# Performance work log

Measured on AMD Instinct MI355X. Metric: run time of the kernel, lower is better.

The kernel has to match this reference:

```python
import jax, jax.numpy as jnp
import numpy as np

B, T, C, H = 4, 4096, 512, 64

def setup_inputs() -> dict:
    key = jax.random.key(0)
    kx, kk, kq, kv = jax.random.split(key, 4)
    return {
        "x": jax.random.normal(kx, (B, T, C), dtype=jnp.float32),
        "Wk": jax.random.normal(kk, (C, H), dtype=jnp.float32) * (C ** -0.5),
        "Wq": jax.random.normal(kq, (C, H), dtype=jnp.float32) * (C ** -0.5),
        "Wv": jax.random.normal(kv, (C, H), dtype=jnp.float32) * (C ** -0.5),
    }

def reference(x, Wk, Wq, Wv):
    # x: [B, T, C]; bias-free projections to head_size H
    k = x @ Wk  # [B, T, H]
    q = x @ Wq  # [B, T, H]
    v = x @ Wv  # [B, T, H]
    channels = x.shape[-1]
    # NOTE: original scales by channels**-0.5 (embedding dim), not head_size
    scale = jnp.asarray(channels, x.dtype) ** -0.5
    wei = jnp.einsum("bth,bsh->bts", q, k) * scale  # [B, T, T]
    t = x.shape[1]
    causal = jnp.tril(jnp.ones((t, t), dtype=bool))
    wei = jnp.where(causal, wei, -jnp.inf)
    wei = jax.nn.softmax(wei, axis=-1)
    out = jnp.einsum("bts,bsh->bth", wei, v)  # [B, T, H]
    return out
```

## Files before the change

kernel.cpp:

```cpp
#include <hip/hip_runtime.h>


typedef __attribute__((ext_vector_type(8))) __bf16 bf16x8;
typedef __attribute__((ext_vector_type(8))) unsigned short u16x8;
typedef __attribute__((ext_vector_type(4))) float f32x4;

#define B_ 4
#define T_ 4096
#define C_ 512
#define H_ 64
#define BT (B_ * T_)

#define QSCALE (0.04419417382415922f * 1.4426950408889634f)

__device__ __forceinline__ unsigned short f2bf(float f) {
    unsigned int u = __builtin_bit_cast(unsigned int, f);
    u += 0x7fffu + ((u >> 16) & 1u);
    return (unsigned short)(u >> 16);
}

__device__ __forceinline__ unsigned int pkbf(float hi, float lo) {
    return __builtin_amdgcn_perm(__builtin_bit_cast(unsigned int, hi),
                                 __builtin_bit_cast(unsigned int, lo), 0x07060302u);
}

__device__ __forceinline__ f32x4 mfma16(bf16x8 a, bf16x8 b, f32x4 c) {
    return __builtin_amdgcn_mfma_f32_16x16x32_bf16(a, b, c, 0, 0, 0);
}

__global__ __launch_bounds__(256) void wt_kernel(const float* __restrict__ Wk,
                                                 const float* __restrict__ Wq,
                                                 const float* __restrict__ Wv,
                                                 unsigned short* __restrict__ Wtp) {
    int gid = blockIdx.x * 256 + threadIdx.x;
    int fidx = gid >> 9;
    int li = gid & 511;
    int lane = li >> 3, j = li & 7;
    int m3 = fidx / 64;
    int rem = fidx & 63;
    int nt = rem >> 4, kc = rem & 15;
    int h = nt * 16 + (lane & 15);
    int c = kc * 32 + (lane >> 4) * 8 + j;
    const float* W = (m3 == 0) ? Wk : ((m3 == 1) ? Wq : Wv);
    Wtp[gid] = f2bf(W[c * H_ + h]);
}

__global__ __launch_bounds__(256, 4) void proj_kernel(const float* __restrict__ x,
                                                      const unsigned short* __restrict__ Wtp,
                                                      unsigned short* __restrict__ Kf,
                                                      unsigned short* __restrict__ Qf,
                                                      unsigned short* __restrict__ Vf) {
    __shared__ __align__(16) char smem[3 * 64 * 52 * 4];
    float* Mg = (float*)smem;
    unsigned short* Ks_l = (unsigned short*)smem;
    unsigned short* Qs_l = Ks_l + 16 * 68;
    unsigned short* Vt_l = Qs_l + 16 * 68;

    const int tid = threadIdx.x;
    const int t0 = blockIdx.x * 16;
    const int wave = tid >> 6;
    const int lane = tid & 63;
    const int lane15 = lane & 15;
    const int quad = lane >> 4;

    f32x4 acc[12];
#pragma unroll
    for (int i = 0; i < 12; ++i) acc[i] = (f32x4){0.f, 0.f, 0.f, 0.f};

    const float* xrow = x + (long)(t0 + lane15) * C_;

#pragma unroll
    for (int kk = 0; kk < 4; ++kk) {
        const int kc = wave * 4 + kk;
        const float4 a0 = *(const float4*)(xrow + kc * 32 + quad * 8);
        const float4 a1 = *(const float4*)(xrow + kc * 32 + quad * 8 + 4);
        u16x8 t;
        t[0] = f2bf(a0.x); t[1] = f2bf(a0.y); t[2] = f2bf(a0.z); t[3] = f2bf(a0.w);
        t[4] = f2bf(a1.x); t[5] = f2bf(a1.y); t[6] = f2bf(a1.z); t[7] = f2bf(a1.w);
        bf16x8 a = __builtin_bit_cast(bf16x8, t);
#pragma unroll
        for (int m3 = 0; m3 < 3; ++m3) {
#pragma unroll
            for (int nt = 0; nt < 4; ++nt) {
                const bf16x8 b = *(const bf16x8*)&Wtp[(((m3 * 4 + nt) * 16 + kc) << 9) + lane * 8];
                acc[m3 * 4 + nt] = mfma16(a, b, acc[m3 * 4 + nt]);
            }
        }
    }

    if (wave > 0) {
        float* mg = Mg + ((wave - 1) * 64 + lane) * 52;
#pragma unroll
        for (int i = 0; i < 12; ++i) *(f32x4*)(mg + i * 4) = acc[i];
    }
    __syncthreads();
    if (wave == 0) {
#pragma unroll
        for (int w = 0; w < 3; ++w) {
            const float* mg = Mg + (w * 64 + lane) * 52;
#pragma unroll
            for (int i = 0; i < 12; ++i) acc[i] += *(const f32x4*)(mg + i * 4);
        }
    }
    __syncthreads();

    if (wave == 0) {
#pragma unroll
        for (int nt = 0; nt < 4; ++nt) {
            int col = nt * 16 + lane15;
#pragma unroll
            for (int r = 0; r < 4; ++r) {
                int row_l = quad * 4 + r;
                Ks_l[row_l * 68 + col] = f2bf(acc[0 * 4 + nt][r]);
                Qs_l[row_l * 68 + col] = f2bf(acc[1 * 4 + nt][r] * QSCALE);
                Vt_l[col * 18 + row_l] = f2bf(acc[2 * 4 + nt][r]);
            }
        }
    }
    __syncthreads();

    const int b = t0 >> 12;
    const int tloc = t0 & 4095;
    const long gs = (long)(b * 256 + (tloc >> 4));

    {
        const unsigned short* src = (wave < 2) ? Ks_l : Qs_l;
        unsigned short* dst = (wave < 2) ? Kf : Qf;
        const int kk = wave & 1;
        bf16x8 v = *(const bf16x8*)&src[lane15 * 68 + kk * 32 + quad * 8];
        *(bf16x8*)&dst[(gs * 2 + kk) * 512 + lane * 8] = v;
    }
    {
        const int tl16 = (tloc >> 4) & 3;
        const int kkv = tl16 >> 1;
        if ((quad >> 1) == (tl16 & 1)) {
            bf16x8 v = *(const bf16x8*)&Vt_l[(wave * 16 + lane15) * 18 + (quad & 1) * 8];
            const long sb = (long)(b * 64 + (tloc >> 6));
            *(bf16x8*)&Vf[(sb * 8 + wave * 2 + kkv) * 512 + lane * 8] = v;
        }
    }
}

#define PSP 72

__global__ __launch_bounds__(256, 4) void attn_kernel(const unsigned short* __restrict__ Qf,
                                                      const unsigned short* __restrict__ Kf,
                                                      const unsigned short* __restrict__ Vf,
                                                      float* __restrict__ Op,
                                                      float* __restrict__ lp) {
    __shared__ __align__(16) unsigned short Ps[4 * 16 * PSP];

    const int tid = threadIdx.x;
    const int wave = tid >> 6;
    const int lane = tid & 63;
    const int lane15 = lane & 15;
    const int quad = lane >> 4;
    const int b = blockIdx.y;

    const int z = blockIdx.x;
    int g, zb;
    if (z < 16)      { g = 0; zb = 0; }
    else if (z < 48) { g = 1; zb = 16; }
    else if (z < 96) { g = 2; zb = 48; }
    else             { g = 3; zb = 96; }
    const int idx = z - zb;
    const int qt = g * 16 + idx / (g + 1);
    const int chunk = idx % (g + 1);
    const int ntt = min(16, qt + 1 - chunk * 16);
    const int t0k = chunk * 16;

    const long gs_q = (long)(b * 256 + qt * 4 + wave);
    const unsigned short* qb = Qf + gs_q * 1024 + lane * 8;
    const bf16x8 qf0 = *(const bf16x8*)qb;
    const bf16x8 qf1 = *(const bf16x8*)(qb + 512);

    f32x4 o_acc[4];
    float l_acc = 0.f;
#pragma unroll
    for (int hf = 0; hf < 4; ++hf) o_acc[hf] = (f32x4){0.f, 0.f, 0.f, 0.f};

    unsigned short* pw = Ps + wave * 16 * PSP;

    bf16x8 kf[8], vf[8];
    {
        const int kc = t0k;
        const unsigned short* kb = Kf + (long)(b * 256 + kc * 4) * 1024 + lane * 8;
        const unsigned short* vb = Vf + (long)(b * 64 + kc) * 4096 + lane * 8;
#pragma unroll
        for (int ct = 0; ct < 4; ++ct) {
            kf[ct * 2 + 0] = *(const bf16x8*)(kb + ct * 1024);
            kf[ct * 2 + 1] = *(const bf16x8*)(kb + ct * 1024 + 512);
        }
#pragma unroll
        for (int f = 0; f < 8; ++f) vf[f] = *(const bf16x8*)(vb + f * 512);
    }

    for (int t = 0; t < ntt; ++t) {
        const int kc = t0k + t;
        const int tn = (t + 1 < ntt) ? (t + 1) : t;
        const int kcn = t0k + tn;
        const unsigned short* kbn = Kf + (long)(b * 256 + kcn * 4) * 1024 + lane * 8;
        const unsigned short* vbn = Vf + (long)(b * 64 + kcn) * 4096 + lane * 8;

        f32x4 st[4];
#pragma unroll
        for (int ct = 0; ct < 4; ++ct) {
            f32x4 zz = (f32x4){0.f, 0.f, 0.f, 0.f};
            zz = mfma16(kf[ct * 2 + 0], qf0, zz);
            zz = mfma16(kf[ct * 2 + 1], qf1, zz);
            st[ct] = zz;
        }

#pragma unroll
        for (int ct = 0; ct < 4; ++ct) {
            kf[ct * 2 + 0] = *(const bf16x8*)(kbn + ct * 1024);
            kf[ct * 2 + 1] = *(const bf16x8*)(kbn + ct * 1024 + 512);
        }

        if (kc == qt) {
            const int qg = wave * 16 + lane15;
#pragma unroll
            for (int ct = 0; ct < 4; ++ct) {
                const int sb = ct * 16 + quad * 4;
#pragma unroll
                for (int r = 0; r < 4; ++r)
                    if (sb + r > qg) st[ct][r] = -3.0e38f;
            }
        }

#pragma unroll
        for (int ct = 0; ct < 4; ++ct)
#pragma unroll
            for (int r = 0; r < 4; ++r) {
                float p = __builtin_amdgcn_exp2f(st[ct][r]);
                st[ct][r] = p;
                l_acc += p;
            }

#pragma unroll
        for (int ct = 0; ct < 4; ++ct) {
            unsigned int w0 = pkbf(st[ct][1], st[ct][0]);
            unsigned int w1 = pkbf(st[ct][3], st[ct][2]);
            *(uint2*)&pw[lane15 * PSP + ct * 16 + quad * 4] = make_uint2(w0, w1);
        }

        bf16x8 pa0 = *(const bf16x8*)&pw[lane15 * PSP + quad * 8];
        bf16x8 pa1 = *(const bf16x8*)&pw[lane15 * PSP + 32 + quad * 8];
#pragma unroll
        for (int hf = 0; hf < 4; ++hf) {
            o_acc[hf] = mfma16(pa0, vf[hf * 2 + 0], o_acc[hf]);
            o_acc[hf] = mfma16(pa1, vf[hf * 2 + 1], o_acc[hf]);
        }

#pragma unroll
        for (int f = 0; f < 8; ++f) vf[f] = *(const bf16x8*)(vbn + f * 512);
    }

    l_acc += __shfl_xor(l_acc, 16);
    l_acc += __shfl_xor(l_acc, 32);

    const long pbase = ((long)(b * 64 + qt) * 4 + chunk) * 64;
    if (quad == 0) lp[pbase + wave * 16 + lane15] = l_acc;
    float* op = Op + (pbase + wave * 16) * 64;
#pragma unroll
    for (int hf = 0; hf < 4; ++hf)
#pragma unroll
        for (int r = 0; r < 4; ++r)
            op[(quad * 4 + r) * 64 + hf * 16 + lane15] = o_acc[hf][r];
}

__global__ __launch_bounds__(256) void merge_kernel(const float* __restrict__ Op,
                                                    const float* __restrict__ lp,
                                                    float* __restrict__ out) {
    const int qt = blockIdx.x;
    const int b = blockIdx.y;
    const int nc = 1 + (qt >> 4);
    const int tid = threadIdx.x;
    const int row = tid >> 2;
    const int seg = (tid & 3) << 4;

    const long base = (long)(b * 64 + qt) * 4;
    float l = 0.f;
    f32x4 a[4];
#pragma unroll
    for (int j = 0; j < 4; ++j) a[j] = (f32x4){0.f, 0.f, 0.f, 0.f};

    for (int c = 0; c < nc; ++c) {
        l += lp[(base + c) * 64 + row];
        const float* op = Op + ((base + c) * 64 + row) * 64 + seg;
#pragma unroll
        for (int j = 0; j < 4; ++j) a[j] += *(const f32x4*)(op + j * 4);
    }
    const float inv = 1.0f / l;
    float* o = out + ((long)b * T_ + qt * 64 + row) * H_ + seg;
#pragma unroll
    for (int j = 0; j < 4; ++j) *(f32x4*)(o + j * 4) = a[j] * inv;
}

extern "C" void kernel_launch(void* const* d_in, const int* in_sizes, int n_in,
                              void* d_out, int out_size, void* d_ws, size_t ws_size,
                              hipStream_t stream) {
    const float* x  = (const float*)d_in[0];
    const float* Wk = (const float*)d_in[1];
    const float* Wq = (const float*)d_in[2];
    const float* Wv = (const float*)d_in[3];
    float* out = (float*)d_out;

    char* ws = (char*)d_ws;
    unsigned short* Kf  = (unsigned short*)(ws);
    unsigned short* Qf  = (unsigned short*)(ws + (2u << 20));
    unsigned short* Vf  = (unsigned short*)(ws + (4u << 20));
    unsigned short* Wtp = (unsigned short*)(ws + (6u << 20));
    float* Op = (float*)(ws + (8u << 20));
    float* lp = (float*)(ws + (24u << 20));

    wt_kernel<<<384, 256, 0, stream>>>(Wk, Wq, Wv, Wtp);
    proj_kernel<<<BT / 16, 256, 0, stream>>>(x, Wtp, Kf, Qf, Vf);
    attn_kernel<<<dim3(160, B_), 256, 0, stream>>>(Qf, Kf, Vf, Op, lp);
    merge_kernel<<<dim3(64, B_), 256, 0, stream>>>(Op, lp, out);
}
```

Before: 120.3 us.

## Retile projection to 32 rows, reverse attention block order, skip merge for single-chunk tiles

The projection kernel now handles 32 tokens per block with a 2x2 wave split over tokens and K halves. It software-pipelines the x and weight loads into registers and halves the shared-memory reduction. The attention kernel launches its blocks in reverse order so the longest query tiles start first, and it drops the redundant next-tile prefetch on the last iteration. Query tiles with a single chunk now normalize and write the output directly, so the merge kernel only handles the remaining 48 tiles. Occupancy hints drop from 4 to 3 waves per SIMD, which trades occupancy for more registers and may change latency hiding.

Measured after the change: 120.5 us. Within noise of the previous version (+0.2%).

```diff
diff --git a/kernel.cpp b/kernel.cpp
--- a/kernel.cpp
+++ b/kernel.cpp
@@ -45,20 +45,22 @@
     Wtp[gid] = f2bf(W[c * H_ + h]);
 }
 
-__global__ __launch_bounds__(256, 4) void proj_kernel(const float* __restrict__ x,
+__global__ __launch_bounds__(256, 3) void proj_kernel(const float* __restrict__ x,
                                                       const unsigned short* __restrict__ Wtp,
                                                       unsigned short* __restrict__ Kf,
                                                       unsigned short* __restrict__ Qf,
                                                       unsigned short* __restrict__ Vf) {
-    __shared__ __align__(16) char smem[3 * 64 * 52 * 4];
+    __shared__ __align__(16) char smem[2 * 64 * 52 * 4];
     float* Mg = (float*)smem;
     unsigned short* Ks_l = (unsigned short*)smem;
-    unsigned short* Qs_l = Ks_l + 16 * 68;
-    unsigned short* Vt_l = Qs_l + 16 * 68;
+    unsigned short* Qs_l = Ks_l + 32 * 68;
+    unsigned short* Vt_l = Qs_l + 32 * 68;
 
     const int tid = threadIdx.x;
-    const int t0 = blockIdx.x * 16;
+    const int t0 = blockIdx.x * 32;
     const int wave = tid >> 6;
+    const int ws = wave & 1;
+    const int wh = wave >> 1;
     const int lane = tid & 63;
     const int lane15 = lane & 15;
     const int quad = lane >> 4;
@@ -67,53 +69,62 @@
 #pragma unroll
     for (int i = 0; i < 12; ++i) acc[i] = (f32x4){0.f, 0.f, 0.f, 0.f};
 
-    const float* xrow = x + (long)(t0 + lane15) * C_;
-
-#pragma unroll
-    for (int kk = 0; kk < 4; ++kk) {
-        const int kc = wave * 4 + kk;
-        const float4 a0 = *(const float4*)(xrow + kc * 32 + quad * 8);
-        const float4 a1 = *(const float4*)(xrow + kc * 32 + quad * 8 + 4);
+    const float* xrow = x + (long)(t0 + ws * 16 + lane15) * C_;
+    const unsigned short* wbase = Wtp + lane * 8;
+
+    bf16x8 wf[12];
+    float4 xa0, xa1;
+    {
+        const int kc0 = wh * 8;
+        xa0 = *(const float4*)(xrow + kc0 * 32 + quad * 8);
+        xa1 = *(const float4*)(xrow + kc0 * 32 + quad * 8 + 4);
+#pragma unroll
+        for (int i = 0; i < 12; ++i)
+            wf[i] = *(const bf16x8*)(wbase + ((i * 16 + kc0) << 9));
+    }
+
+#pragma unroll
+    for (int kk = 0; kk < 8; ++kk) {
+        const int kc = wh * 8 + kk;
         u16x8 t;
-        t[0] = f2bf(a0.x); t[1] = f2bf(a0.y); t[2] = f2bf(a0.z); t[3] = f2bf(a0.w);
-        t[4] = f2bf(a1.x); t[5] = f2bf(a1.y); t[6] = f2bf(a1.z); t[7] = f2bf(a1.w);
+        t[0] = f2bf(xa0.x); t[1] = f2bf(xa0.y); t[2] = f2bf(xa0.z); t[3] = f2bf(xa0.w);
+        t[4] = f2bf(xa1.x); t[5] = f2bf(xa1.y); t[6] = f2bf(xa1.z); t[7] = f2bf(xa1.w);
         bf16x8 a = __builtin_bit_cast(bf16x8, t);
-#pragma unroll
-        for (int m3 = 0; m3 < 3; ++m3) {
-#pragma unroll
-            for (int nt = 0; nt < 4; ++nt) {
-                const bf16x8 b = *(const bf16x8*)&Wtp[(((m3 * 4 + nt) * 16 + kc) << 9) + lane * 8];
-                acc[m3 * 4 + nt] = mfma16(a, b, acc[m3 * 4 + nt]);
-            }
-        }
-    }
-
-    if (wave > 0) {
-        float* mg = Mg + ((wave - 1) * 64 + lane) * 52;
+        if (kk < 7) {
+            xa0 = *(const float4*)(xrow + (kc + 1) * 32 + quad * 8);
+            xa1 = *(const float4*)(xrow + (kc + 1) * 32 + quad * 8 + 4);
+        }
+#pragma unroll
+        for (int i = 0; i < 12; ++i) {
+            acc[i] = mfma16(a, wf[i], acc[i]);
+            if (kk < 7)
+                wf[i] = *(const bf16x8*)(wbase + ((i * 16 + kc + 1) << 9));
+        }
+    }
+
+    if (wh == 1) {
+        float* mg = Mg + (ws * 64 + lane) * 52;
 #pragma unroll
         for (int i = 0; i < 12; ++i) *(f32x4*)(mg + i * 4) = acc[i];
     }
     __syncthreads();
-    if (wave == 0) {
-#pragma unroll
-        for (int w = 0; w < 3; ++w) {
-            const float* mg = Mg + (w * 64 + lane) * 52;
-#pragma unroll
-            for (int i = 0; i < 12; ++i) acc[i] += *(const f32x4*)(mg + i * 4);
-        }
+    if (wh == 0) {
+        const float* mg = Mg + (ws * 64 + lane) * 52;
+#pragma unroll
+        for (int i = 0; i < 12; ++i) acc[i] += *(const f32x4*)(mg + i * 4);
     }
     __syncthreads();
 
-    if (wave == 0) {
+    if (wh == 0) {
 #pragma unroll
         for (int nt = 0; nt < 4; ++nt) {
             int col = nt * 16 + lane15;
 #pragma unroll
             for (int r = 0; r < 4; ++r) {
-                int row_l = quad * 4 + r;
+                int row_l = ws * 16 + quad * 4 + r;
                 Ks_l[row_l * 68 + col] = f2bf(acc[0 * 4 + nt][r]);
                 Qs_l[row_l * 68 + col] = f2bf(acc[1 * 4 + nt][r] * QSCALE);
-                Vt_l[col * 18 + row_l] = f2bf(acc[2 * 4 + nt][r]);
+                Vt_l[col * 34 + row_l] = f2bf(acc[2 * 4 + nt][r]);
             }
         }
     }
@@ -121,33 +132,27 @@
 
     const int b = t0 >> 12;
     const int tloc = t0 & 4095;
-    const long gs = (long)(b * 256 + (tloc >> 4));
-
-    {
-        const unsigned short* src = (wave < 2) ? Ks_l : Qs_l;
-        unsigned short* dst = (wave < 2) ? Kf : Qf;
-        const int kk = wave & 1;
-        bf16x8 v = *(const bf16x8*)&src[lane15 * 68 + kk * 32 + quad * 8];
-        *(bf16x8*)&dst[(gs * 2 + kk) * 512 + lane * 8] = v;
-    }
-    {
-        const int tl16 = (tloc >> 4) & 3;
-        const int kkv = tl16 >> 1;
-        if ((quad >> 1) == (tl16 & 1)) {
-            bf16x8 v = *(const bf16x8*)&Vt_l[(wave * 16 + lane15) * 18 + (quad & 1) * 8];
-            const long sb = (long)(b * 64 + (tloc >> 6));
-            *(bf16x8*)&Vf[(sb * 8 + wave * 2 + kkv) * 512 + lane * 8] = v;
-        }
-    }
+    const int st = wave >> 1, kk = wave & 1;
+    const long gs = (long)(b * 256 + (tloc >> 4) + st);
+    bf16x8 kv = *(const bf16x8*)&Ks_l[(st * 16 + lane15) * 68 + kk * 32 + quad * 8];
+    *(bf16x8*)&Kf[(gs * 2 + kk) * 512 + lane * 8] = kv;
+    bf16x8 qv = *(const bf16x8*)&Qs_l[(st * 16 + lane15) * 68 + kk * 32 + quad * 8];
+    *(bf16x8*)&Qf[(gs * 2 + kk) * 512 + lane * 8] = qv;
+    const int hf = wave;
+    const int vkk = (tloc >> 5) & 1;
+    bf16x8 vv = *(const bf16x8*)&Vt_l[(hf * 16 + lane15) * 34 + quad * 8];
+    const long sb = (long)(b * 64 + (tloc >> 6));
+    *(bf16x8*)&Vf[(sb * 8 + hf * 2 + vkk) * 512 + lane * 8] = vv;
 }
 
 #define PSP 72
 
-__global__ __launch_bounds__(256, 4) void attn_kernel(const unsigned short* __restrict__ Qf,
+__global__ __launch_bounds__(256, 3) void attn_kernel(const unsigned short* __restrict__ Qf,
                                                       const unsigned short* __restrict__ Kf,
                                                       const unsigned short* __restrict__ Vf,
                                                       float* __restrict__ Op,
-                                                      float* __restrict__ lp) {
+                                                      float* __restrict__ lp,
+                                                      float* __restrict__ out) {
     __shared__ __align__(16) unsigned short Ps[4 * 16 * PSP];
 
     const int tid = threadIdx.x;
@@ -157,7 +162,7 @@
     const int quad = lane >> 4;
     const int b = blockIdx.y;
 
-    const int z = blockIdx.x;
+    const int z = 159 - blockIdx.x;
     int g, zb;
     if (z < 16)      { g = 0; zb = 0; }
     else if (z < 48) { g = 1; zb = 16; }
@@ -183,9 +188,8 @@
 
     bf16x8 kf[8], vf[8];
     {
-        const int kc = t0k;
-        const unsigned short* kb = Kf + (long)(b * 256 + kc * 4) * 1024 + lane * 8;
-        const unsigned short* vb = Vf + (long)(b * 64 + kc) * 4096 + lane * 8;
+        const unsigned short* kb = Kf + (long)(b * 256 + t0k * 4) * 1024 + lane * 8;
+        const unsigned short* vb = Vf + (long)(b * 64 + t0k) * 4096 + lane * 8;
 #pragma unroll
         for (int ct = 0; ct < 4; ++ct) {
             kf[ct * 2 + 0] = *(const bf16x8*)(kb + ct * 1024);
@@ -197,10 +201,9 @@
 
     for (int t = 0; t < ntt; ++t) {
         const int kc = t0k + t;
-        const int tn = (t + 1 < ntt) ? (t + 1) : t;
-        const int kcn = t0k + tn;
-        const unsigned short* kbn = Kf + (long)(b * 256 + kcn * 4) * 1024 + lane * 8;
-        const unsigned short* vbn = Vf + (long)(b * 64 + kcn) * 4096 + lane * 8;
+        const bool more = (t + 1 < ntt);
+        const unsigned short* kbn = Kf + (long)(b * 256 + (kc + 1) * 4) * 1024 + lane * 8;
+        const unsigned short* vbn = Vf + (long)(b * 64 + kc + 1) * 4096 + lane * 8;
 
         f32x4 st[4];
 #pragma unroll
@@ -211,10 +214,12 @@
             st[ct] = zz;
         }
 
-#pragma unroll
-        for (int ct = 0; ct < 4; ++ct) {
-            kf[ct * 2 + 0] = *(const bf16x8*)(kbn + ct * 1024);
-            kf[ct * 2 + 1] = *(const bf16x8*)(kbn + ct * 1024 + 512);
+        if (more) {
+#pragma unroll
+            for (int ct = 0; ct < 4; ++ct) {
+                kf[ct * 2 + 0] = *(const bf16x8*)(kbn + ct * 1024);
+                kf[ct * 2 + 1] = *(const bf16x8*)(kbn + ct * 1024 + 512);
+            }
         }
 
         if (kc == qt) {
@@ -252,27 +257,41 @@
             o_acc[hf] = mfma16(pa1, vf[hf * 2 + 1], o_acc[hf]);
         }
 
-#pragma unroll
-        for (int f = 0; f < 8; ++f) vf[f] = *(const bf16x8*)(vbn + f * 512);
+        if (more) {
+#pragma unroll
+            for (int f = 0; f < 8; ++f) vf[f] = *(const bf16x8*)(vbn + f * 512);
+        }
     }
 
     l_acc += __shfl_xor(l_acc, 16);
     l_acc += __shfl_xor(l_acc, 32);
 
-    const long pbase = ((long)(b * 64 + qt) * 4 + chunk) * 64;
-    if (quad == 0) lp[pbase + wave * 16 + lane15] = l_acc;
-    float* op = Op + (pbase + wave * 16) * 64;
-#pragma unroll
-    for (int hf = 0; hf < 4; ++hf)
-#pragma unroll
-        for (int r = 0; r < 4; ++r)
-            op[(quad * 4 + r) * 64 + hf * 16 + lane15] = o_acc[hf][r];
+    if ((qt >> 4) == 0) {
+        float linv[4];
+#pragma unroll
+        for (int r = 0; r < 4; ++r) linv[r] = 1.0f / __shfl(l_acc, quad * 4 + r);
+        float* o = out + ((long)b * T_ + qt * 64 + wave * 16) * H_;
+#pragma unroll
+        for (int hf = 0; hf < 4; ++hf)
+#pragma unroll
+            for (int r = 0; r < 4; ++r)
+                o[(quad * 4 + r) * H_ + hf * 16 + lane15] = o_acc[hf][r] * linv[r];
+    } else {
+        const long pbase = ((long)(b * 64 + qt) * 4 + chunk) * 64;
+        if (quad == 0) lp[pbase + wave * 16 + lane15] = l_acc;
+        float* op = Op + (pbase + wave * 16) * 64;
+#pragma unroll
+        for (int hf = 0; hf < 4; ++hf)
+#pragma unroll
+            for (int r = 0; r < 4; ++r)
+                op[(quad * 4 + r) * 64 + hf * 16 + lane15] = o_acc[hf][r];
+    }
 }
 
 __global__ __launch_bounds__(256) void merge_kernel(const float* __restrict__ Op,
                                                     const float* __restrict__ lp,
                                                     float* __restrict__ out) {
-    const int qt = blockIdx.x;
+    const int qt = 16 + blockIdx.x;
     const int b = blockIdx.y;
     const int nc = 1 + (qt >> 4);
     const int tid = threadIdx.x;
@@ -315,7 +334,7 @@
     float* lp = (float*)(ws + (24u << 20));
 
     wt_kernel<<<384, 256, 0, stream>>>(Wk, Wq, Wv, Wtp);
-    proj_kernel<<<BT / 16, 256, 0, stream>>>(x, Wtp, Kf, Qf, Vf);
-    attn_kernel<<<dim3(160, B_), 256, 0, stream>>>(Qf, Kf, Vf, Op, lp);
-    merge_kernel<<<dim3(64, B_), 256, 0, stream>>>(Op, lp, out);
-}
+    proj_kernel<<<BT / 32, 256, 0, stream>>>(x, Wtp, Kf, Qf, Vf);
+    attn_kernel<<<dim3(160, B_), 256, 0, stream>>>(Qf, Kf, Vf, Op, lp, out);
+    merge_kernel<<<dim3(48, B_), 256, 0, stream>>>(Op, lp, out);
+}
```
